# Kernel tuning notes

Hardware: AMD Instinct MI355X
Metric: run time of the kernel (lower is better)

Reference implementation:

```python
import jax, jax.numpy as jnp
import numpy as np

D = 1024          # hidden_dim
H = 16            # num_heads
G = 32            # number of graphs in the batch
N = 512           # nodes per graph (equal-size graphs -> the per-graph loop becomes one batched attention)
T = G * N         # total nodes
EPS = 1e-5


def _layernorm(x, g, b):
    mu = jnp.mean(x, axis=-1, keepdims=True)
    var = jnp.mean(jnp.square(x - mu), axis=-1, keepdims=True)
    return (x - mu) * jax.lax.rsqrt(var + EPS) * g + b


def setup_inputs() -> dict:
    key = jax.random.key(0)
    ks = jax.random.split(key, 10)
    s = 0.02
    inp = {
        "h": jax.random.normal(ks[0], (T, D), dtype=jnp.float32),
        "w_in": jax.random.normal(ks[1], (3 * D, D), dtype=jnp.float32) * s,   # MHA in_proj_weight
        "b_in": jnp.zeros((3 * D,), dtype=jnp.float32),
        "w_out": jax.random.normal(ks[2], (D, D), dtype=jnp.float32) * s,      # MHA out_proj
        "b_out": jnp.zeros((D,), dtype=jnp.float32),
        "ln1_g": jnp.ones((D,), dtype=jnp.float32),
        "ln1_b": jnp.zeros((D,), dtype=jnp.float32),
        "ln2_g": jnp.ones((D,), dtype=jnp.float32),
        "ln2_b": jnp.zeros((D,), dtype=jnp.float32),
        "ffn_w1": jax.random.normal(ks[3], (2 * D, D), dtype=jnp.float32) * s,
        "ffn_b1": jnp.zeros((2 * D,), dtype=jnp.float32),
        "ffn_w2": jax.random.normal(ks[4], (D, 2 * D), dtype=jnp.float32) * s,
        "ffn_b2": jnp.zeros((D,), dtype=jnp.float32),
        "edge_index": jax.random.randint(ks[5], (2, 65536), 0, T, dtype=jnp.int64),
        "batch": jnp.repeat(jnp.arange(G, dtype=jnp.int64), N),
        "num_graphs": G,
    }
    return inp


def reference(h, w_in, b_in, w_out, b_out, ln1_g, ln1_b, ln2_g, ln2_b,
              ffn_w1, ffn_b1, ffn_w2, ffn_b2, edge_index, batch, num_graphs):
    # Per-graph self-attention: equal-size contiguous graphs -> reshape to [G, N, D]
    hd = D // H
    x = h.reshape(num_graphs, -1, D)                       # [G, N, D]
    n = x.shape[1]
    qkv = x @ w_in.T + b_in                                # [G, N, 3D]
    q, k, v = jnp.split(qkv, 3, axis=-1)
    q = q.reshape(num_graphs, n, H, hd).transpose(0, 2, 1, 3)  # [G, H, N, hd]
    k = k.reshape(num_graphs, n, H, hd).transpose(0, 2, 1, 3)
    v = v.reshape(num_graphs, n, H, hd).transpose(0, 2, 1, 3)
    scores = jnp.einsum('ghnd,ghmd->ghnm', q, k) / np.sqrt(hd)
    attn = jax.nn.softmax(scores, axis=-1)
    o = jnp.einsum('ghnm,ghmd->ghnd', attn, v)             # [G, H, N, hd]
    o = o.transpose(0, 2, 1, 3).reshape(num_graphs, n, D)
    o = o @ w_out.T + b_out
    x = _layernorm(x + o, ln1_g, ln1_b)                    # residual + norm1
    f = jax.nn.relu(x @ ffn_w1.T + ffn_b1) @ ffn_w2.T + ffn_b2  # dropout: eval mode (identity)
    x = _layernorm(x + f, ln2_g, ln2_b)                    # residual + norm2
    return x.reshape(-1, D)                                # [T, D]
```

## Files before the change

kernel.cpp:

```cpp
#include <hip/hip_runtime.h>
#include <stdint.h>

typedef unsigned short u16;
typedef __attribute__((ext_vector_type(8))) short bf16x8;
typedef __attribute__((ext_vector_type(4))) float f32x4;

#define AS1C(p) ((const __attribute__((address_space(1))) char*)(const char*)(p))
#define AS3C(p) ((__attribute__((address_space(3))) char*)(char*)(p))

static __device__ __forceinline__ u16 f2bf(float f) {
  uint32_t u = __builtin_bit_cast(uint32_t, f);
  u = (u + 0x7FFFu + ((u >> 16) & 1u)) >> 16;
  return (u16)u;
}

__global__ __launch_bounds__(256) void k_f2bf(const float* __restrict__ src,
                                              u16* __restrict__ dst, int n4) {
  int i = blockIdx.x * blockDim.x + threadIdx.x;
  if (i >= n4) return;
  float4 v = reinterpret_cast<const float4*>(src)[i];
  ushort4 o;
  o.x = f2bf(v.x); o.y = f2bf(v.y); o.z = f2bf(v.z); o.w = f2bf(v.w);
  reinterpret_cast<ushort4*>(dst)[i] = o;
}

template<bool OUT_BF16, bool RELU>
__global__ __launch_bounds__(256) void k_gemm(const u16* __restrict__ A,
                                              const u16* __restrict__ B,
                                              const float* __restrict__ bias,
                                              void* __restrict__ C,
                                              int M, int N, int K) {
  __shared__ __align__(16) char As[8192];
  __shared__ __align__(16) char Bs[8192];
  const int tid  = threadIdx.x;
  const int lane = tid & 63;
  const int wid  = tid >> 6;
  const int wm = wid >> 1, wn = wid & 1;
  const long bm = (long)blockIdx.y * 128, bn = (long)blockIdx.x * 128;

  const int o0 = wid * 2048 + lane * 16;
  const int o1 = o0 + 1024;
  const int r0 = o0 >> 6, kb0 = o0 & 63;
  const int r1 = o1 >> 6, kb1 = o1 & 63;
  const unsigned l0 = (unsigned)__builtin_amdgcn_readfirstlane(wid * 2048);
  const unsigned l1 = l0 + 1024;
  const char* Ab = (const char*)A;
  const char* Bb = (const char*)B;

  f32x4 acc[4][4];
#pragma unroll
  for (int i = 0; i < 4; i++)
#pragma unroll
    for (int j = 0; j < 4; j++) acc[i][j] = 0.f;

  const int nK = K >> 5;
  for (int kt = 0; kt < nK; ++kt) {
    const long k0 = (long)kt * 32;
    __builtin_amdgcn_global_load_lds(AS1C(Ab + ((bm + r0) * K + k0) * 2 + kb0), AS3C(As + l0), 16, 0, 0);
    __builtin_amdgcn_global_load_lds(AS1C(Ab + ((bm + r1) * K + k0) * 2 + kb1), AS3C(As + l1), 16, 0, 0);
    __builtin_amdgcn_global_load_lds(AS1C(Bb + ((bn + r0) * K + k0) * 2 + kb0), AS3C(Bs + l0), 16, 0, 0);
    __builtin_amdgcn_global_load_lds(AS1C(Bb + ((bn + r1) * K + k0) * 2 + kb1), AS3C(Bs + l1), 16, 0, 0);
    __syncthreads();
    bf16x8 af[4], bfr[4];
#pragma unroll
    for (int i = 0; i < 4; i++) {
      af[i]  = *reinterpret_cast<const bf16x8*>(As + (wm * 64 + i * 16 + (lane & 15)) * 64 + (lane >> 4) * 16);
      bfr[i] = *reinterpret_cast<const bf16x8*>(Bs + (wn * 64 + i * 16 + (lane & 15)) * 64 + (lane >> 4) * 16);
    }
#pragma unroll
    for (int i = 0; i < 4; i++)
#pragma unroll
      for (int j = 0; j < 4; j++)
        acc[i][j] = __builtin_amdgcn_mfma_f32_16x16x32_bf16(af[i], bfr[j], acc[i][j], 0, 0, 0);
    __syncthreads();
  }

  u16* Cb = (u16*)C;
  float* Cf = (float*)C;
#pragma unroll
  for (int j = 0; j < 4; j++) {
    const long col = bn + wn * 64 + j * 16 + (lane & 15);
    const float bv = bias[col];
#pragma unroll
    for (int i = 0; i < 4; i++) {
      const long rbase = bm + wm * 64 + i * 16 + (lane >> 4) * 4;
#pragma unroll
      for (int q = 0; q < 4; q++) {
        float v = acc[i][j][q] + bv;
        if (RELU) v = fmaxf(v, 0.f);
        if (OUT_BF16) Cb[(rbase + q) * N + col] = f2bf(v);
        else          Cf[(rbase + q) * N + col] = v;
      }
    }
  }
}

__global__ __launch_bounds__(256) void k_transpose_v(const u16* __restrict__ qkv,
                                                     u16* __restrict__ vt) {
  const int gh = blockIdx.x, g = gh >> 4, h = gh & 15;
  const int tid = threadIdx.x;
  __shared__ __align__(16) u16 tile[4096];
  for (int nt = 0; nt < 8; ++nt) {
    const int n0 = nt * 64;
#pragma unroll
    for (int c = 0; c < 2; ++c) {
      const int ch = tid * 2 + c;
      const int n = ch >> 3;
      const int cc = ch & 7;
      const uint4 v = *reinterpret_cast<const uint4*>(
          qkv + (long)(g * 512 + n0 + n) * 3072 + 2048 + h * 64 + cc * 8);
      const int phys = cc ^ (n & 7) ^ (n >> 3);
      *reinterpret_cast<uint4*>(tile + n * 64 + phys * 8) = v;
    }
    __syncthreads();
#pragma unroll
    for (int c = 0; c < 2; ++c) {
      const int ch = tid * 2 + c;
      const int crow = ch >> 3;
      const int noff = (ch & 7) * 8;
      union { u16 s[8]; uint4 u; } val;
#pragma unroll
      for (int i = 0; i < 8; ++i) {
        const int n = noff + i;
        const int phys = (crow >> 3) ^ (n & 7) ^ (n >> 3);
        val.s[i] = tile[n * 64 + phys * 8 + (crow & 7)];
      }
      *reinterpret_cast<uint4*>(vt + (long)(gh * 64 + crow) * 512 + n0 + noff) = val.u;
    }
    __syncthreads();
  }
}

__global__ __launch_bounds__(256) void k_attn(const u16* __restrict__ qkv,
                                              const u16* __restrict__ vt,
                                              u16* __restrict__ out) {
  __shared__ __align__(16) char Ks[8192];
  __shared__ __align__(16) char Vs[8192];
  __shared__ __align__(16) char Ps[4][2048];
  const int tid = threadIdx.x, lane = tid & 63, wid = tid >> 6;
  const int qb = blockIdx.x, h = blockIdx.y, g = blockIdx.z;
  const int gh = g * 16 + h;
  const long grow0 = (long)g * 512;
  const char* qbase = (const char*)qkv;

  const long qrow = qb * 64 + wid * 16 + (lane & 15);
  bf16x8 qf[2];
#pragma unroll
  for (int kf = 0; kf < 2; ++kf) {
    const long go = (((grow0 + qrow) * 3072) + h * 64 + kf * 32 + (lane >> 4) * 8) * 2;
    qf[kf] = *reinterpret_cast<const bf16x8*>(qbase + go);
  }

  f32x4 oacc[4];
#pragma unroll
  for (int i = 0; i < 4; i++) oacc[i] = 0.f;
  float mrun[4], lrun[4];
#pragma unroll
  for (int q = 0; q < 4; q++) { mrun[q] = -3.0e38f; lrun[q] = 0.f; }

  const unsigned l0 = (unsigned)__builtin_amdgcn_readfirstlane(wid * 2048);
  const unsigned l1 = l0 + 1024;

  for (int it = 0; it < 8; ++it) {
    const int kv0 = it * 64;
#pragma unroll
    for (int c = 0; c < 2; ++c) {
      const int o = wid * 2048 + c * 1024 + lane * 16;
      const int row = o >> 7;
      const int pch = (o >> 4) & 7;
      const int lch = pch ^ (row & 7);
      const long gK = (((grow0 + kv0 + row) * 3072) + 1024 + h * 64 + lch * 8) * 2;
      __builtin_amdgcn_global_load_lds(AS1C(qbase + gK), AS3C(Ks + (c ? l1 : l0)), 16, 0, 0);
      const long gV = (((long)(gh * 64 + row)) * 512 + kv0 + lch * 8) * 2;
      __builtin_amdgcn_global_load_lds(AS1C((const char*)vt + gV), AS3C(Vs + (c ? l1 : l0)), 16, 0, 0);
    }
    __syncthreads();

    f32x4 s[4];
#pragma unroll
    for (int nt = 0; nt < 4; ++nt) {
      const int krow = nt * 16 + (lane & 15);
      const int sw = krow & 7;
      const bf16x8 k0 = *reinterpret_cast<const bf16x8*>(Ks + krow * 128 + (((lane >> 4)) ^ sw) * 16);
      const bf16x8 k1 = *reinterpret_cast<const bf16x8*>(Ks + krow * 128 + (((lane >> 4) + 4) ^ sw) * 16);
      f32x4 t = 0.f;
      t = __builtin_amdgcn_mfma_f32_16x16x32_bf16(qf[0], k0, t, 0, 0, 0);
      t = __builtin_amdgcn_mfma_f32_16x16x32_bf16(qf[1], k1, t, 0, 0, 0);
#pragma unroll
      for (int q = 0; q < 4; q++) t[q] *= 0.125f;
      s[nt] = t;
    }

    float tmax[4];
#pragma unroll
    for (int q = 0; q < 4; q++)
      tmax[q] = fmaxf(fmaxf(s[0][q], s[1][q]), fmaxf(s[2][q], s[3][q]));
#pragma unroll
    for (int d = 1; d < 16; d <<= 1)
#pragma unroll
      for (int q = 0; q < 4; q++) tmax[q] = fmaxf(tmax[q], __shfl_xor(tmax[q], d));
    float sf[4];
#pragma unroll
    for (int q = 0; q < 4; q++) {
      const float mn = fmaxf(mrun[q], tmax[q]);
      sf[q] = __expf(mrun[q] - mn);
      mrun[q] = mn;
    }
    float rs[4] = {0.f, 0.f, 0.f, 0.f};
#pragma unroll
    for (int nt = 0; nt < 4; nt++)
#pragma unroll
      for (int q = 0; q < 4; q++) {
        const float p = __expf(s[nt][q] - mrun[q]);
        s[nt][q] = p;
        rs[q] += p;
      }
#pragma unroll
    for (int d = 1; d < 16; d <<= 1)
#pragma unroll
      for (int q = 0; q < 4; q++) rs[q] += __shfl_xor(rs[q], d);
#pragma unroll
    for (int q = 0; q < 4; q++) lrun[q] = lrun[q] * sf[q] + rs[q];
#pragma unroll
    for (int i = 0; i < 4; i++)
#pragma unroll
      for (int q = 0; q < 4; q++) oacc[i][q] *= sf[q];

    char* pw = Ps[wid];
#pragma unroll
    for (int nt = 0; nt < 4; nt++) {
      const int cc = nt * 16 + (lane & 15);
#pragma unroll
      for (int q = 0; q < 4; q++) {
        const int r = (lane >> 4) * 4 + q;
        const int phys = (cc >> 3) ^ (r & 7);
        *(u16*)(pw + r * 128 + phys * 16 + (cc & 7) * 2) = f2bf(s[nt][q]);
      }
    }

#pragma unroll
    for (int kf = 0; kf < 2; ++kf) {
      const int prow = lane & 15;
      const bf16x8 pa = *reinterpret_cast<const bf16x8*>(
          pw + prow * 128 + ((kf * 4 + (lane >> 4)) ^ (prow & 7)) * 16);
#pragma unroll
      for (int ot = 0; ot < 4; ++ot) {
        const int vr = ot * 16 + (lane & 15);
        const bf16x8 vb = *reinterpret_cast<const bf16x8*>(
            Vs + vr * 128 + ((kf * 4 + (lane >> 4)) ^ (vr & 7)) * 16);
        oacc[ot] = __builtin_amdgcn_mfma_f32_16x16x32_bf16(pa, vb, oacc[ot], 0, 0, 0);
      }
    }
    __syncthreads();
  }

#pragma unroll
  for (int ot = 0; ot < 4; ++ot) {
    const int col = h * 64 + ot * 16 + (lane & 15);
#pragma unroll
    for (int q = 0; q < 4; q++) {
      const long r = grow0 + qb * 64 + wid * 16 + (lane >> 4) * 4 + q;
      out[r * 1024 + col] = f2bf(oacc[ot][q] / lrun[q]);
    }
  }
}

template<bool EMIT_BF16>
__global__ __launch_bounds__(256) void k_ln(const float* __restrict__ A,
                                            const float* __restrict__ Bz,
                                            const float* __restrict__ gam,
                                            const float* __restrict__ bet,
                                            float* __restrict__ out_f,
                                            u16* __restrict__ out_b) {
  const int row = blockIdx.x;
  const int tid = threadIdx.x;
  const long base = (long)row * 1024;
  const float4 a = reinterpret_cast<const float4*>(A + base)[tid];
  const float4 b = reinterpret_cast<const float4*>(Bz + base)[tid];
  const float x0 = a.x + b.x, x1 = a.y + b.y, x2 = a.z + b.z, x3 = a.w + b.w;
  float s1 = x0 + x1 + x2 + x3;
  float s2 = x0 * x0 + x1 * x1 + x2 * x2 + x3 * x3;
#pragma unroll
  for (int d = 1; d < 64; d <<= 1) { s1 += __shfl_xor(s1, d); s2 += __shfl_xor(s2, d); }
  __shared__ float red[8];
  const int wid = tid >> 6, lane = tid & 63;
  if (lane == 0) { red[wid] = s1; red[4 + wid] = s2; }
  __syncthreads();
  s1 = red[0] + red[1] + red[2] + red[3];
  s2 = red[4] + red[5] + red[6] + red[7];
  const float mu = s1 * (1.f / 1024.f);
  const float var = s2 * (1.f / 1024.f) - mu * mu;
  const float rstd = rsqrtf(var + 1e-5f);
  const float4 gv = reinterpret_cast<const float4*>(gam)[tid];
  const float4 bv = reinterpret_cast<const float4*>(bet)[tid];
  float4 y;
  y.x = (x0 - mu) * rstd * gv.x + bv.x;
  y.y = (x1 - mu) * rstd * gv.y + bv.y;
  y.z = (x2 - mu) * rstd * gv.z + bv.z;
  y.w = (x3 - mu) * rstd * gv.w + bv.w;
  reinterpret_cast<float4*>(out_f + base)[tid] = y;
  if (EMIT_BF16) {
    ushort4 o;
    o.x = f2bf(y.x); o.y = f2bf(y.y); o.z = f2bf(y.z); o.w = f2bf(y.w);
    reinterpret_cast<ushort4*>(out_b + base)[tid] = o;
  }
}

extern "C" void kernel_launch(void* const* d_in, const int* in_sizes, int n_in,
                              void* d_out, int out_size, void* d_ws, size_t ws_size,
                              hipStream_t stream) {
  const float* h    = (const float*)d_in[0];
  const float* w_in = (const float*)d_in[1];
  const float* b_in = (const float*)d_in[2];
  const float* w_o  = (const float*)d_in[3];
  const float* b_o  = (const float*)d_in[4];
  const float* ln1g = (const float*)d_in[5];
  const float* ln1b = (const float*)d_in[6];
  const float* ln2g = (const float*)d_in[7];
  const float* ln2b = (const float*)d_in[8];
  const float* w1   = (const float*)d_in[9];
  const float* b1   = (const float*)d_in[10];
  const float* w2   = (const float*)d_in[11];
  const float* b2   = (const float*)d_in[12];

  const size_t WS_NEED = 184549376;
  if (ws_size < WS_NEED) {
    hipMemsetAsync(d_out, 0, (size_t)out_size * 4, stream);
    return;
  }

  char* W = (char*)d_ws;
  u16* h_bf     = (u16*)(W + 0);
  u16* w_in_bf  = (u16*)(W + 33554432);
  u16* w_out_bf = (u16*)(W + 39845888);
  u16* w1_bf    = (u16*)(W + 41943040);
  u16* w2_bf    = (u16*)(W + 46137344);
  u16* qkv      = (u16*)(W + 50331648);
  u16* vt       = (u16*)(W + 150994944);
  float* x1     = (float*)(W + 50331648);
  u16* f1       = (u16*)(W + 117440512);
  u16* attn_bf  = h_bf;
  u16* x1_bf    = h_bf;
  float* o32    = (float*)d_out;
  float* f2     = (float*)d_out;

  k_f2bf<<<dim3(16384), 256, 0, stream>>>(h, h_bf, 4194304);
  k_f2bf<<<dim3(3072),  256, 0, stream>>>(w_in, w_in_bf, 786432);
  k_f2bf<<<dim3(1024),  256, 0, stream>>>(w_o, w_out_bf, 262144);
  k_f2bf<<<dim3(2048),  256, 0, stream>>>(w1, w1_bf, 524288);
  k_f2bf<<<dim3(2048),  256, 0, stream>>>(w2, w2_bf, 524288);

  k_gemm<true, false><<<dim3(24, 128), 256, 0, stream>>>(h_bf, w_in_bf, b_in, (void*)qkv, 16384, 3072, 1024);
  k_transpose_v<<<dim3(512), 256, 0, stream>>>(qkv, vt);
  k_attn<<<dim3(8, 16, 32), 256, 0, stream>>>(qkv, vt, attn_bf);
  k_gemm<false, false><<<dim3(8, 128), 256, 0, stream>>>(attn_bf, w_out_bf, b_o, (void*)o32, 16384, 1024, 1024);
  k_ln<true><<<dim3(16384), 256, 0, stream>>>(h, o32, ln1g, ln1b, x1, x1_bf);
  k_gemm<true, true><<<dim3(16, 128), 256, 0, stream>>>(x1_bf, w1_bf, b1, (void*)f1, 16384, 2048, 1024);
  k_gemm<false, false><<<dim3(8, 128), 256, 0, stream>>>(f1, w2_bf, b2, (void*)f2, 16384, 1024, 2048);
  k_ln<false><<<dim3(16384), 256, 0, stream>>>(x1, f2, ln2g, ln2b, (float*)d_out, (u16*)nullptr);
}
```

Baseline: 809.2 us.

## Replace GEMM with 256x256-tile double-buffered pipelined MFMA kernel

Replaces the 128x128 single-buffered GEMM with a 256x256 tile, 512-thread kernel. It double-buffers 64-wide K slices in 128KB of LDS, uses an XOR-swizzled LDS layout, remaps blocks for L2-friendly XCD grouping, and interleaves global-to-LDS loads with MFMA phases using explicit waitcnt, barriers and setprio. The aim is to hide memory latency and raise arithmetic intensity in the four dense projections. In exchange it needs many more registers and lots of LDS, which limits occupancy. It also relies on hand-tuned barrier and waitcnt ordering, which is fragile.

```diff
diff --git a/kernel.cpp b/kernel.cpp
--- a/kernel.cpp
+++ b/kernel.cpp
@@ -24,75 +24,125 @@
   reinterpret_cast<ushort4*>(dst)[i] = o;
 }
 
+#define BAR()  do { asm volatile("" ::: "memory"); __builtin_amdgcn_s_barrier(); asm volatile("" ::: "memory"); } while (0)
+#define WLG()  asm volatile("s_waitcnt lgkmcnt(0)" ::: "memory")
+#define WV4()  asm volatile("s_waitcnt vmcnt(4)" ::: "memory")
+
 template<bool OUT_BF16, bool RELU>
-__global__ __launch_bounds__(256) void k_gemm(const u16* __restrict__ A,
-                                              const u16* __restrict__ B,
-                                              const float* __restrict__ bias,
-                                              void* __restrict__ C,
-                                              int M, int N, int K) {
-  __shared__ __align__(16) char As[8192];
-  __shared__ __align__(16) char Bs[8192];
-  const int tid  = threadIdx.x;
-  const int lane = tid & 63;
-  const int wid  = tid >> 6;
-  const int wm = wid >> 1, wn = wid & 1;
-  const long bm = (long)blockIdx.y * 128, bn = (long)blockIdx.x * 128;
-
-  const int o0 = wid * 2048 + lane * 16;
-  const int o1 = o0 + 1024;
-  const int r0 = o0 >> 6, kb0 = o0 & 63;
-  const int r1 = o1 >> 6, kb1 = o1 & 63;
-  const unsigned l0 = (unsigned)__builtin_amdgcn_readfirstlane(wid * 2048);
-  const unsigned l1 = l0 + 1024;
-  const char* Ab = (const char*)A;
-  const char* Bb = (const char*)B;
-
-  f32x4 acc[4][4];
-#pragma unroll
-  for (int i = 0; i < 4; i++)
-#pragma unroll
-    for (int j = 0; j < 4; j++) acc[i][j] = 0.f;
-
-  const int nK = K >> 5;
-  for (int kt = 0; kt < nK; ++kt) {
-    const long k0 = (long)kt * 32;
-    __builtin_amdgcn_global_load_lds(AS1C(Ab + ((bm + r0) * K + k0) * 2 + kb0), AS3C(As + l0), 16, 0, 0);
-    __builtin_amdgcn_global_load_lds(AS1C(Ab + ((bm + r1) * K + k0) * 2 + kb1), AS3C(As + l1), 16, 0, 0);
-    __builtin_amdgcn_global_load_lds(AS1C(Bb + ((bn + r0) * K + k0) * 2 + kb0), AS3C(Bs + l0), 16, 0, 0);
-    __builtin_amdgcn_global_load_lds(AS1C(Bb + ((bn + r1) * K + k0) * 2 + kb1), AS3C(Bs + l1), 16, 0, 0);
-    __syncthreads();
-    bf16x8 af[4], bfr[4];
-#pragma unroll
-    for (int i = 0; i < 4; i++) {
-      af[i]  = *reinterpret_cast<const bf16x8*>(As + (wm * 64 + i * 16 + (lane & 15)) * 64 + (lane >> 4) * 16);
-      bfr[i] = *reinterpret_cast<const bf16x8*>(Bs + (wn * 64 + i * 16 + (lane & 15)) * 64 + (lane >> 4) * 16);
-    }
-#pragma unroll
-    for (int i = 0; i < 4; i++)
-#pragma unroll
-      for (int j = 0; j < 4; j++)
-        acc[i][j] = __builtin_amdgcn_mfma_f32_16x16x32_bf16(af[i], bfr[j], acc[i][j], 0, 0, 0);
-    __syncthreads();
-  }
+__global__ __launch_bounds__(512, 2) void k_gemm256(const u16* __restrict__ A,
+                                                    const u16* __restrict__ B,
+                                                    const float* __restrict__ bias,
+                                                    void* __restrict__ C,
+                                                    int M, int N, int K) {
+  __shared__ __align__(16) char lds[131072];
+  const int tid = threadIdx.x, lane = tid & 63, wid = tid >> 6;
+  const int wm = wid >> 2, wn = wid & 3;
+
+  const int nbx = N >> 8;
+  const int cpx = gridDim.x >> 3;
+  const int sid = ((int)blockIdx.x & 7) * cpx + ((int)blockIdx.x >> 3);
+  const int bm = (sid / nbx) << 8;
+  const int bn = (sid % nbx) << 8;
+
+  int ga[2], gb[2];
+  unsigned wdst[2];
+#pragma unroll
+  for (int c = 0; c < 2; ++c) {
+    const int o = wid * 2048 + c * 1024 + lane * 16;
+    const int r = o >> 7;
+    const int kb = (((o >> 4) & 7) ^ (r & 7)) * 16;
+    ga[c] = (bm + r) * K * 2 + kb;
+    gb[c] = (bn + r) * K * 2 + kb;
+    wdst[c] = (unsigned)__builtin_amdgcn_readfirstlane(wid * 2048 + c * 1024);
+  }
+  const int hStep = 128 * K * 2;
+  const char* Ag = (const char*)A;
+  const char* Bg = (const char*)B;
+
+  const int rA = (wm * 128 + (lane & 15)) * 128;
+  const int rB = 32768 + (wn * 64 + (lane & 15)) * 128;
+  int ck[2];
+#pragma unroll
+  for (int s = 0; s < 2; ++s) ck[s] = ((s * 4 + (lane >> 4)) ^ (lane & 7)) * 16;
+
+  f32x4 acc[8][4];
+#pragma unroll
+  for (int m = 0; m < 8; ++m)
+#pragma unroll
+    for (int n = 0; n < 4; ++n) acc[m][n] = 0.f;
+  bf16x8 am[4][2], b0f[2][2], b1f[2][2];
+
+#define STG(isB, half, t, buf) do { \
+  _Pragma("unroll") for (int c_ = 0; c_ < 2; ++c_) { \
+    const char* s_ = ((isB) ? Bg : Ag) + ((isB) ? gb[c_] : ga[c_]) + (half) * hStep + (t) * 128; \
+    __builtin_amdgcn_global_load_lds(AS1C(s_), \
+        AS3C(lds + ((buf) * 65536 + (isB) * 32768 + (half) * 16384 + wdst[c_])), 16, 0, 0); \
+  } } while (0)
+
+#define RDA(buf, mh) do { \
+  _Pragma("unroll") for (int m_ = 0; m_ < 4; ++m_) \
+  _Pragma("unroll") for (int s_ = 0; s_ < 2; ++s_) \
+    am[m_][s_] = *(const bf16x8*)(lds + (buf) * 65536 + rA + ((mh) * 64 + m_ * 16) * 128 + ck[s_]); } while (0)
+
+#define RDB(buf, nh, dst) do { \
+  _Pragma("unroll") for (int n_ = 0; n_ < 2; ++n_) \
+  _Pragma("unroll") for (int s_ = 0; s_ < 2; ++s_) \
+    dst[n_][s_] = *(const bf16x8*)(lds + (buf) * 65536 + rB + ((nh) * 32 + n_ * 16) * 128 + ck[s_]); } while (0)
+
+#define MM(mh, nh, bf) do { \
+  __builtin_amdgcn_s_setprio(1); \
+  _Pragma("unroll") for (int m_ = 0; m_ < 4; ++m_) \
+  _Pragma("unroll") for (int n_ = 0; n_ < 2; ++n_) \
+  _Pragma("unroll") for (int s_ = 0; s_ < 2; ++s_) \
+    acc[(mh) * 4 + m_][(nh) * 2 + n_] = __builtin_amdgcn_mfma_f32_16x16x32_bf16( \
+        am[m_][s_], bf[n_][s_], acc[(mh) * 4 + m_][(nh) * 2 + n_], 0, 0, 0); \
+  __builtin_amdgcn_s_setprio(0); } while (0)
+
+  const int nT = K >> 6, tmask = nT - 1, nIter = K >> 7;
+
+  STG(1, 0, 0, 0); STG(1, 1, 0, 0); STG(0, 0, 0, 0); STG(0, 1, 0, 0);
+  STG(1, 0, 1, 1); STG(1, 1, 1, 1);
+  WV4();
+  BAR();
+
+  for (int i = 0; i < nIter; ++i) {
+    const int t1 = 2 * i + 1;
+    const int t2 = (2 * i + 2) & tmask;
+    const int t3 = (2 * i + 3) & tmask;
+    RDA(0, 0); RDB(0, 0, b0f); STG(0, 0, t1, 1); BAR(); WLG(); MM(0, 0, b0f); BAR();
+    RDB(0, 1, b1f); STG(0, 1, t1, 1); BAR(); WLG(); MM(0, 1, b1f); BAR();
+    RDA(0, 1); STG(1, 0, t2, 0); BAR(); WLG(); MM(1, 1, b1f); BAR();
+    STG(1, 1, t2, 0); WV4(); BAR(); MM(1, 0, b0f); BAR();
+    RDA(1, 0); RDB(1, 0, b0f); STG(0, 0, t2, 0); BAR(); WLG(); MM(0, 0, b0f); BAR();
+    RDB(1, 1, b1f); STG(0, 1, t2, 0); BAR(); WLG(); MM(0, 1, b1f); BAR();
+    RDA(1, 1); STG(1, 0, t3, 1); BAR(); WLG(); MM(1, 1, b1f); BAR();
+    STG(1, 1, t3, 1); WV4(); BAR(); MM(1, 0, b0f); BAR();
+  }
+  asm volatile("s_waitcnt vmcnt(0)" ::: "memory");
 
   u16* Cb = (u16*)C;
   float* Cf = (float*)C;
 #pragma unroll
-  for (int j = 0; j < 4; j++) {
-    const long col = bn + wn * 64 + j * 16 + (lane & 15);
+  for (int n = 0; n < 4; ++n) {
+    const int col = bn + wn * 64 + n * 16 + (lane & 15);
     const float bv = bias[col];
 #pragma unroll
-    for (int i = 0; i < 4; i++) {
-      const long rbase = bm + wm * 64 + i * 16 + (lane >> 4) * 4;
-#pragma unroll
-      for (int q = 0; q < 4; q++) {
-        float v = acc[i][j][q] + bv;
+    for (int m = 0; m < 8; ++m) {
+      const int rbase = bm + wm * 128 + m * 16 + (lane >> 4) * 4;
+#pragma unroll
+      for (int q = 0; q < 4; ++q) {
+        float v = acc[m][n][q] + bv;
         if (RELU) v = fmaxf(v, 0.f);
-        if (OUT_BF16) Cb[(rbase + q) * N + col] = f2bf(v);
-        else          Cf[(rbase + q) * N + col] = v;
+        const long idx = (long)(rbase + q) * N + col;
+        if (OUT_BF16) Cb[idx] = f2bf(v);
+        else          Cf[idx] = v;
       }
     }
   }
+#undef STG
+#undef RDA
+#undef RDB
+#undef MM
 }
 
 __global__ __launch_bounds__(256) void k_transpose_v(const u16* __restrict__ qkv,
@@ -350,12 +400,12 @@
   k_f2bf<<<dim3(2048),  256, 0, stream>>>(w1, w1_bf, 524288);
   k_f2bf<<<dim3(2048),  256, 0, stream>>>(w2, w2_bf, 524288);
 
-  k_gemm<true, false><<<dim3(24, 128), 256, 0, stream>>>(h_bf, w_in_bf, b_in, (void*)qkv, 16384, 3072, 1024);
+  k_gemm256<true, false><<<dim3(768), 512, 0, stream>>>(h_bf, w_in_bf, b_in, (void*)qkv, 16384, 3072, 1024);
   k_transpose_v<<<dim3(512), 256, 0, stream>>>(qkv, vt);
   k_attn<<<dim3(8, 16, 32), 256, 0, stream>>>(qkv, vt, attn_bf);
-  k_gemm<false, false><<<dim3(8, 128), 256, 0, stream>>>(attn_bf, w_out_bf, b_o, (void*)o32, 16384, 1024, 1024);
+  k_gemm256<false, false><<<dim3(256), 512, 0, stream>>>(attn_bf, w_out_bf, b_o, (void*)o32, 16384, 1024, 1024);
   k_ln<true><<<dim3(16384), 256, 0, stream>>>(h, o32, ln1g, ln1b, x1, x1_bf);
-  k_gemm<true, true><<<dim3(16, 128), 256, 0, stream>>>(x1_bf, w1_bf, b1, (void*)f1, 16384, 2048, 1024);
-  k_gemm<false, false><<<dim3(8, 128), 256, 0, stream>>>(f1, w2_bf, b2, (void*)f2, 16384, 1024, 2048);
+  k_gemm256<true, true><<<dim3(512), 512, 0, stream>>>(x1_bf, w1_bf, b1, (void*)f1, 16384, 2048, 1024);
+  k_gemm256<false, false><<<dim3(256), 512, 0, stream>>>(f1, w2_bf, b2, (void*)f2, 16384, 1024, 2048);
   k_ln<false><<<dim3(16384), 256, 0, stream>>>(x1, f2, ln2g, ln2b, (float*)d_out, (u16*)nullptr);
 }
```

New measurement: 684.7 us. 15.4% less time.
